# Optimization experiments

Measured on AMD Instinct MI355X. Metric: run time of the kernel, lower is better.

## Reference

```python
import jax, jax.numpy as jnp
import numpy as np

B, P, D = 16, 512, 1024   # batch, num wordpieces, bert_dim (roberta-large)
W, T, E = 400, 32, 64     # num words, num triggers (spans), num entities (spans)
H = 600                   # hidden_num of role_idn_ffn


def _make_idxs(rng, b, m, n, max_len):
    # [start, end) intervals with 0 <= start < end <= n, sorted starts per row
    starts = np.sort(rng.integers(0, n - 1, size=(b, m)), axis=1)
    ends = np.minimum(starts + rng.integers(1, max_len + 1, size=(b, m)), n)
    ends = np.maximum(ends, starts + 1)
    return np.stack([starts, ends], axis=-1).astype(np.int32)


def setup_inputs() -> dict:
    key = jax.random.key(0)
    k1, k2, k3 = jax.random.split(key, 3)
    rng = np.random.default_rng(0)
    return {
        "piece_reprs": jax.random.normal(k1, (B, P, D), dtype=jnp.float32),
        "word_idxs": jnp.asarray(_make_idxs(rng, B, W, P, 4)),
        "trigger_idxs": jnp.asarray(_make_idxs(rng, B, T, W, 8)),
        "entity_idxs": jnp.asarray(_make_idxs(rng, B, E, W, 12)),
        "W0": jax.random.normal(k2, (4 * D, H), dtype=jnp.float32) * 0.02,
        "b0": jnp.zeros((H,), dtype=jnp.float32),
        "W1": jax.random.normal(k3, (H, 2), dtype=jnp.float32) * 0.02,
        "b1": jnp.zeros((2,), dtype=jnp.float32),
    }


def _segment_mean(x, idxs):
    """Mean of x[b, start:end] per interval. x: [B,N,Dm], idxs: [B,M,2] -> [B,M,Dm].
    Vectorized replacement of the nested-loop slice+mean via inclusive prefix sums."""
    cs = jnp.concatenate([jnp.zeros_like(x[:, :1]), jnp.cumsum(x, axis=1)], axis=1)  # [B,N+1,Dm]
    s = jnp.take_along_axis(cs, idxs[:, :, 0:1], axis=1)  # [B,M,Dm]
    e = jnp.take_along_axis(cs, idxs[:, :, 1:2], axis=1)  # [B,M,Dm]
    lens = (idxs[:, :, 1] - idxs[:, :, 0]).astype(x.dtype)[:, :, None]
    return (e - s) / lens


def reference(piece_reprs, word_idxs, trigger_idxs, entity_idxs, W0, b0, W1, b1):
    # encode(): wordpiece -> word averaging (compute_word_reps_avg)
    word_reprs = _segment_mean(piece_reprs, word_idxs)          # [B, W, D]
    # scores(): span mean pooling (compute_span_reprs)
    trig = _segment_mean(word_reprs, trigger_idxs)              # [B, T, D]
    ent = _segment_mean(word_reprs, entity_idxs)                # [B, E, D]
    b, t, d = trig.shape
    e = ent.shape[1]
    # compute_binary_reprs: all (trigger, entity) pairs, trigger index varies slowly
    t_rep = jnp.broadcast_to(trig[:, :, None, :], (b, t, e, d)).reshape(b, t * e, d)
    e_rep = jnp.broadcast_to(ent[:, None, :, :], (b, t, e, d)).reshape(b, t * e, d)
    role = jnp.concatenate([t_rep, e_rep, t_rep * e_rep, jnp.abs(t_rep - e_rep)], axis=-1)  # [B,T*E,4D]
    # role_idn_ffn: Linears([4D, H, 2]) with relu between layers (dropout=0 at eval)
    h = jax.nn.relu(role @ W0 + b0)
    return h @ W1 + b1                                          # [B, T*E, 2]
```

## Files before the change

### kernel.cpp

```cpp
#include <hip/hip_runtime.h>
#include <cstddef>
#include <cstdint>

typedef float f32x4 __attribute__((ext_vector_type(4)));
typedef __bf16 bf16x8 __attribute__((ext_vector_type(8)));

constexpr int NB = 16;
constexpr int NP = 512;
constexpr int ND = 1024;
constexpr int NW = 400;
constexpr int NT = 32;
constexpr int NE = 64;
constexpr int NH = 600;
constexpr int IMGP = 128 * 64;
constexpr int IMGQ = 320 * 32;
constexpr int PREZ_N = NB * NT * NH + NB * NE * NH;

__device__ inline bf16x8 pack8(float a0, float a1, float a2, float a3,
                               float a4, float a5, float a6, float a7) {
    bf16x8 v;
    v[0] = (__bf16)a0; v[1] = (__bf16)a1; v[2] = (__bf16)a2; v[3] = (__bf16)a3;
    v[4] = (__bf16)a4; v[5] = (__bf16)a5; v[6] = (__bf16)a6; v[7] = (__bf16)a7;
    return v;
}

__device__ inline void dma16(const void* g, void* l) {
    __builtin_amdgcn_global_load_lds(
        (const __attribute__((address_space(1))) uint32_t*)g,
        (__attribute__((address_space(3))) uint32_t*)l, 16, 0, 0);
}

#define LGKM_BARRIER() \
    asm volatile("s_waitcnt lgkmcnt(0)\n\ts_barrier" ::: "memory")

template <int MAXW>
__device__ inline float4 span_mean_cols(const float* __restrict__ pbase,
                                        const int* __restrict__ wrow,
                                        int s, int e) {
    int nw = e - s;
    int ps[MAXW], pe[MAXW];
#pragma unroll
    for (int w = 0; w < MAXW; ++w) {
        bool act = w < nw;
        int ww = s + w;
        ps[w] = act ? wrow[2 * ww] : 0;
        pe[w] = act ? wrow[2 * ww + 1] : 0;
    }
    float4 acc = make_float4(0.f, 0.f, 0.f, 0.f);
#pragma unroll
    for (int w = 0; w < MAXW; ++w) {
        float4 wa = make_float4(0.f, 0.f, 0.f, 0.f);
#pragma unroll
        for (int p = 0; p < 4; ++p) {
            if (ps[w] + p < pe[w]) {
                float4 v = *(const float4*)(pbase + (size_t)(ps[w] + p) * ND);
                wa.x += v.x; wa.y += v.y; wa.z += v.z; wa.w += v.w;
            }
        }
        if (pe[w] > ps[w]) {
            float wi = 1.0f / (float)(pe[w] - ps[w]);
            acc.x += wa.x * wi; acc.y += wa.y * wi;
            acc.z += wa.z * wi; acc.w += wa.w * wi;
        }
    }
    return acc;
}

__global__ __launch_bounds__(256) void prep_kernel(
    const float* __restrict__ piece, const int* __restrict__ widx,
    const int* __restrict__ tidx, const int* __restrict__ eidx,
    const float* __restrict__ W0, __bf16* __restrict__ W0pre,
    __bf16* __restrict__ W0pair, float* __restrict__ trig,
    float* __restrict__ ent, float* __restrict__ prez,
    float* __restrict__ out, int out_size) {
    __shared__ float T[64][132];
    int id = blockIdx.x;
    int t = threadIdx.x;
    if (id < NB * (NT + NE)) {
        const int* idx;
        float* outp;
        int b;
        bool is_trig = id < NB * NT;
        if (is_trig) {
            b = id / NT; idx = tidx + id * 2; outp = trig + (size_t)id * ND;
        } else {
            int id2 = id - NB * NT;
            b = id2 / NE; idx = eidx + id2 * 2; outp = ent + (size_t)id2 * ND;
        }
        int s = idx[0], e = idx[1];
        int col = t * 4;
        const int* wrow = widx + b * NW * 2;
        const float* pbase = piece + (size_t)b * NP * ND + col;
        float4 acc = is_trig ? span_mean_cols<8>(pbase, wrow, s, e)
                             : span_mean_cols<12>(pbase, wrow, s, e);
        float inv = 1.0f / (float)(e - s);
        acc.x *= inv; acc.y *= inv; acc.z *= inv; acc.w *= inv;
        *(float4*)(outp + col) = acc;
    } else if (id < NB * (NT + NE) + 704) {
        int bid = id - NB * (NT + NE);
        if (bid < 160) {
            int kb = bid & 31, nc = bid >> 5;
            {
                int kl = t >> 2;
                int n0 = (t & 3) * 32;
                int kg = kb * 64 + kl;
                const float* src = W0 + (size_t)kg * NH + nc * 128 + n0;
#pragma unroll
                for (int g = 0; g < 8; ++g) {
                    int n = nc * 128 + n0 + g * 4;
                    float4 v = (n < NH) ? *(const float4*)(src + g * 4)
                                        : make_float4(0.f, 0.f, 0.f, 0.f);
                    *(float4*)&T[kl][n0 + g * 4] = v;
                }
            }
            __syncthreads();
#pragma unroll
            for (int s = 0; s < 4; ++s) {
                int idx = t * 4 + s;
                int row = idx >> 3, c = idx & 7;
                bf16x8 v = pack8(T[c * 8 + 0][row], T[c * 8 + 1][row],
                                 T[c * 8 + 2][row], T[c * 8 + 3][row],
                                 T[c * 8 + 4][row], T[c * 8 + 5][row],
                                 T[c * 8 + 6][row], T[c * 8 + 7][row]);
                __bf16* img = W0pre + ((size_t)nc * 32 + kb) * IMGP;
                *(bf16x8*)&img[row * 64 + ((c ^ (row & 7)) << 3)] = v;
            }
        } else if (bid < 672) {
            int e = bid - 160;
            int it = e & 63, nc = (e >> 6) & 1, zz = e >> 7;
            float (*Tp)[84] = reinterpret_cast<float(*)[84]>(&T[0][0]);
            {
                int kidx = t >> 3, part = t & 7;
                int korig = (kidx < 16) ? (2048 + it * 16 + kidx)
                                        : (3072 + it * 16 + (kidx - 16));
                const float* src = W0 + (size_t)korig * NH;
#pragma unroll
                for (int g = 0; g < 10; ++g) {
                    int n = nc * 320 + zz * 80 + part * 10 + g;
                    Tp[kidx][part * 10 + g] = (n < NH) ? src[n] : 0.0f;
                }
            }
            __syncthreads();
            __bf16* img = W0pair + ((size_t)nc * 64 + it) * IMGQ;
#pragma unroll
            for (int s = 0; s < 2; ++s) {
                int idx = s * 256 + t;
                if (idx < 320) {
                    int rloc = idx >> 2, c = idx & 3;
                    bf16x8 v = pack8(Tp[c * 8 + 0][rloc], Tp[c * 8 + 1][rloc],
                                     Tp[c * 8 + 2][rloc], Tp[c * 8 + 3][rloc],
                                     Tp[c * 8 + 4][rloc], Tp[c * 8 + 5][rloc],
                                     Tp[c * 8 + 6][rloc], Tp[c * 8 + 7][rloc]);
                    int rg = zz * 80 + rloc;
                    int slot = ((rg >> 1) + c) & 3;
                    *(bf16x8*)&img[rg * 32 + slot * 8] = v;
                }
            }
        } else {
            int j = ((bid - 672) * 256 + t) * 8;
            float4 z = make_float4(0.f, 0.f, 0.f, 0.f);
            if (j + 8 <= out_size) {
                *(float4*)(out + j) = z;
                *(float4*)(out + j + 4) = z;
            }
        }
    } else {
        int id2 = id - (NB * (NT + NE) + 704);
        int j = (id2 * 256 + t) * 8;
        float4 z = make_float4(0.f, 0.f, 0.f, 0.f);
        if (j + 8 <= PREZ_N) {
            *(float4*)(prez + j) = z;
            *(float4*)(prez + j + 4) = z;
        }
    }
}

__global__ __launch_bounds__(256) void pre_mfma_kernel(
    const float* __restrict__ trig, const float* __restrict__ ent,
    const __bf16* __restrict__ W0pre, float* __restrict__ pre_t,
    float* __restrict__ pre_e) {
    __shared__ __bf16 As[2][64 * 64];
    __shared__ __bf16 Bs[3][64 * 64];
    int mt8 = blockIdx.x, ntile = blockIdx.y, kz = blockIdx.z;
    const float* A;
    float* C;
    int kbofs, mbase;
    if (mt8 < 8) { A = trig; C = pre_t; kbofs = 0;  mbase = mt8 * 64; }
    else         { A = ent;  C = pre_e; kbofs = 16; mbase = (mt8 - 8) * 64; }
    int tid = threadIdx.x;
    int lane = tid & 63, w = tid >> 6, rw = w & 1, cw = w >> 1;
    int q = lane >> 4, l15 = lane & 15, sa = l15 & 7;
    int nc = ntile >> 1, half = ntile & 1;
    const __bf16* imgbase =
        W0pre + ((size_t)nc * 32 + kbofs) * IMGP + half * 4096;
    int ar = tid >> 2, seg = tid & 3;
    f32x4 acc[2][2] = {};
    float4 av[4];

    auto dma_bb = [&](int it, int buf) {
        const __bf16* img = imgbase + (size_t)(kz * 8 + it) * IMGP;
#pragma unroll
        for (int i = 0; i < 2; ++i) {
            int idx = i * 4 + w;
            dma16(img + idx * 512 + lane * 8, (__bf16*)Bs[buf] + idx * 512);
        }
    };
    auto load_a = [&](int it) {
        const float* src = A + (size_t)(mbase + ar) * ND + (kz * 8 + it) * 64;
#pragma unroll
        for (int i = 0; i < 2; ++i) {
            int c = seg * 2 + i;
            av[i * 2]     = *(const float4*)(src + c * 8);
            av[i * 2 + 1] = *(const float4*)(src + c * 8 + 4);
        }
    };
    auto write_a = [&](int buf) {
#pragma unroll
        for (int i = 0; i < 2; ++i) {
            int c = seg * 2 + i;
            float4 a0 = av[i * 2], a1 = av[i * 2 + 1];
            *(bf16x8*)&As[buf][ar * 64 + ((c ^ (ar & 7)) << 3)] =
                pack8(a0.x, a0.y, a0.z, a0.w, a1.x, a1.y, a1.z, a1.w);
        }
    };
    auto mfma_t = [&](int abuf, int bbuf) {
#pragma unroll
        for (int ks = 0; ks < 2; ++ks) {
            int coff = ((q ^ sa) ^ (ks << 2)) << 3;
            bf16x8 af[2];
#pragma unroll
            for (int mt = 0; mt < 2; ++mt)
                af[mt] = *(const bf16x8*)&As[abuf][(32 * rw + 16 * mt + l15) * 64 + coff];
#pragma unroll
            for (int nt = 0; nt < 2; ++nt) {
                bf16x8 bf = *(const bf16x8*)&Bs[bbuf][(32 * cw + 16 * nt + l15) * 64 + coff];
#pragma unroll
                for (int mt = 0; mt < 2; ++mt)
                    acc[mt][nt] = __builtin_amdgcn_mfma_f32_16x16x32_bf16(
                        af[mt], bf, acc[mt][nt], 0, 0, 0);
            }
        }
    };

    load_a(0);
    dma_bb(0, 0);
    dma_bb(1, 1);
    write_a(0);
    __syncthreads();

    int bc = 0, bp = 2;
    for (int it = 0; it < 8; ++it) {
        int acur = it & 1, anxt = acur ^ 1;
        if (it < 7) load_a(it + 1);
        if (it < 6) dma_bb(it + 2, bp);
        __builtin_amdgcn_s_setprio(1);
        mfma_t(acur, bc);
        __builtin_amdgcn_s_setprio(0);
        if (it < 7) write_a(anxt);
        LGKM_BARRIER();
        bc = (bc == 2) ? 0 : bc + 1;
        bp = (bp == 2) ? 0 : bp + 1;
    }

#pragma unroll
    for (int mt = 0; mt < 2; ++mt)
#pragma unroll
        for (int r = 0; r < 4; ++r) {
            float* crow =
                C + (size_t)(mbase + 32 * rw + 16 * mt + 4 * q + r) * NH;
#pragma unroll
            for (int nt = 0; nt < 2; ++nt) {
                int n = ntile * 64 + 32 * cw + 16 * nt + l15;
                if (n < NH) atomicAdd(&crow[n], acc[mt][nt][r]);
            }
        }
}

__global__ __launch_bounds__(256, 2) void pair_mfma_kernel(
    const float* __restrict__ trig, const float* __restrict__ ent,
    const __bf16* __restrict__ W0pair, const float* __restrict__ b0,
    const float* __restrict__ pre_t, const float* __restrict__ pre_e,
    const float* __restrict__ W1, const float* __restrict__ b1,
    float* __restrict__ out) {
    __shared__ __bf16 Xs[2][128 * 32];
    __shared__ __bf16 Bs[3][320 * 32];
    __shared__ __bf16 Ts[2048];
    int b = blockIdx.x, tp = blockIdx.y, nc = blockIdx.z;
    int tid = threadIdx.x;
    int lane = tid & 63, w = tid >> 6, rw = w & 1, cw = w >> 1;
    int q = lane >> 4, l15 = lane & 15;
    int xr = tid >> 1, xh = tid & 1;
    const float* t0row = trig + (size_t)(b * NT + tp * 2) * ND;
    const float* erow = ent + (size_t)(b * NE + (xr & 63)) * ND;
    const __bf16* imgbase = W0pair + (size_t)nc * 64 * IMGQ;
    f32x4 acc[4][10] = {};
    float4 ef4[2];

    auto dma_b = [&](int it, int buf) {
        const __bf16* img = imgbase + (size_t)it * IMGQ + w * 2560;
        __bf16* lds = &Bs[buf][w * 2560];
#pragma unroll
        for (int i = 0; i < 5; ++i)
            dma16(img + i * 512 + lane * 8, lds + i * 512);
    };
    auto load_e = [&](int it) {
        const float* er = erow + it * 16 + xh * 8;
        ef4[0] = *(const float4*)er;
        ef4[1] = *(const float4*)(er + 4);
    };
    auto write_x = [&](int it, int buf) {
        bf16x8 tv = *(const bf16x8*)&Ts[(xr >> 6) * 1024 + it * 16 + xh * 8];
        float tf[8], ef[8];
#pragma unroll
        for (int j = 0; j < 8; ++j) tf[j] = (float)tv[j];
        ef[0] = ef4[0].x; ef[1] = ef4[0].y; ef[2] = ef4[0].z; ef[3] = ef4[0].w;
        ef[4] = ef4[1].x; ef[5] = ef4[1].y; ef[6] = ef4[1].z; ef[7] = ef4[1].w;
        int sp = (((xr >> 1) + xh) & 3) * 8;
        int sd = (((xr >> 1) + 2 + xh) & 3) * 8;
        __bf16* xb = &Xs[buf][xr * 32];
        *(bf16x8*)(xb + sp) = pack8(
            tf[0] * ef[0], tf[1] * ef[1], tf[2] * ef[2], tf[3] * ef[3],
            tf[4] * ef[4], tf[5] * ef[5], tf[6] * ef[6], tf[7] * ef[7]);
        *(bf16x8*)(xb + sd) = pack8(
            fabsf(tf[0] - ef[0]), fabsf(tf[1] - ef[1]),
            fabsf(tf[2] - ef[2]), fabsf(tf[3] - ef[3]),
            fabsf(tf[4] - ef[4]), fabsf(tf[5] - ef[5]),
            fabsf(tf[6] - ef[6]), fabsf(tf[7] - ef[7]));
    };
    auto mfma_tile = [&](int xbuf, int bbuf) {
        const __bf16* X = Xs[xbuf];
        const __bf16* Bb = Bs[bbuf];
        bf16x8 af[4];
#pragma unroll
        for (int mt = 0; mt < 4; ++mt) {
            int r = 64 * rw + 16 * mt + l15;
            af[mt] = *(const bf16x8*)&X[r * 32 + (((r >> 1) + q) & 3) * 8];
        }
#pragma unroll
        for (int nt = 0; nt < 10; ++nt) {
            int r = 160 * cw + 16 * nt + l15;
            bf16x8 bv = *(const bf16x8*)&Bb[r * 32 + (((r >> 1) + q) & 3) * 8];
#pragma unroll
            for (int mt = 0; mt < 4; ++mt)
                acc[mt][nt] = __builtin_amdgcn_mfma_f32_16x16x32_bf16(
                    af[mt], bv, acc[mt][nt], 0, 0, 0);
        }
    };

    {
        int k0 = (tid & 127) * 8;
        const float* src = t0row + (tid >> 7) * ND + k0;
        float4 va = *(const float4*)src;
        float4 vb = *(const float4*)(src + 4);
        *(bf16x8*)&Ts[tid * 8] =
            pack8(va.x, va.y, va.z, va.w, vb.x, vb.y, vb.z, vb.w);
    }
    dma_b(0, 0);
    load_e(0);
    dma_b(1, 1);
    __syncthreads();
    write_x(0, 0);
    __syncthreads();

    int bc = 0, bp = 2;
    for (int it = 0; it < 64; ++it) {
        int xcur = it & 1, xnxt = xcur ^ 1;
        if (it < 63) load_e(it + 1);
        if (it < 62) dma_b(it + 2, bp);
        __builtin_amdgcn_s_setprio(1);
        mfma_tile(xcur, bc);
        __builtin_amdgcn_s_setprio(0);
        if (it < 63) write_x(it + 1, xnxt);
        LGKM_BARRIER();
        bc = (bc == 2) ? 0 : bc + 1;
        bp = (bp == 2) ? 0 : bp + 1;
    }

    int tglob = b * NT + tp * 2 + rw;
    const float* preT = pre_t + (size_t)tglob * NH;
    float w10[10], w11[10], b0v[10], ptv[10];
    int nbase = nc * 320 + 160 * cw + l15;
#pragma unroll
    for (int nt = 0; nt < 10; ++nt) {
        int n = nbase + 16 * nt;
        bool v = n < NH;
        w10[nt] = v ? W1[2 * n] : 0.f;
        w11[nt] = v ? W1[2 * n + 1] : 0.f;
        b0v[nt] = v ? b0[n] : 0.f;
        ptv[nt] = v ? preT[n] : 0.f;
    }
    float b10 = b1[0], b11 = b1[1];
    bool lead = (l15 == 0);
    bool addb = (nc == 0) && (cw == 0);
#pragma unroll
    for (int mt = 0; mt < 4; ++mt) {
#pragma unroll
        for (int r = 0; r < 4; ++r) {
            int e = 16 * mt + 4 * q + r;
            const float* preE = pre_e + (size_t)(b * NE + e) * NH;
            float s0 = 0.f, s1 = 0.f;
#pragma unroll
            for (int nt = 0; nt < 10; ++nt) {
                int n = nbase + 16 * nt;
                float pe = (n < NH) ? preE[n] : 0.f;
                float h = acc[mt][nt][r] + ptv[nt] + pe + b0v[nt];
                h = fmaxf(h, 0.f);
                s0 += h * w10[nt];
                s1 += h * w11[nt];
            }
#pragma unroll
            for (int m = 8; m >= 1; m >>= 1) {
                s0 += __shfl_xor(s0, m);
                s1 += __shfl_xor(s1, m);
            }
            if (lead) {
                if (addb) { s0 += b10; s1 += b11; }
                float* o = out + ((size_t)(tglob * NE + e)) * 2;
                atomicAdd(o, s0);
                atomicAdd(o + 1, s1);
            }
        }
    }
}

extern "C" void kernel_launch(void* const* d_in, const int* in_sizes, int n_in,
                              void* d_out, int out_size, void* d_ws,
                              size_t ws_size, hipStream_t stream) {
    const float* piece = (const float*)d_in[0];
    const int* widx = (const int*)d_in[1];
    const int* tidx = (const int*)d_in[2];
    const int* eidx = (const int*)d_in[3];
    const float* W0 = (const float*)d_in[4];
    const float* b0 = (const float*)d_in[5];
    const float* W1 = (const float*)d_in[6];
    const float* b1 = (const float*)d_in[7];
    float* out = (float*)d_out;

    float* ws = (float*)d_ws;
    float* trig = ws;
    float* ent = trig + (size_t)NB * NT * ND;
    float* pre_t = ent + (size_t)NB * NE * ND;
    float* pre_e = pre_t + (size_t)NB * NT * NH;
    __bf16* W0pre = (__bf16*)(pre_e + (size_t)NB * NE * NH);
    __bf16* W0pair = W0pre + (size_t)5 * 32 * IMGP;

    int nprep = NB * (NT + NE) + 704 + (PREZ_N / 2048);
    prep_kernel<<<nprep, 256, 0, stream>>>(piece, widx, tidx, eidx, W0, W0pre,
                                           W0pair, trig, ent, pre_t, out,
                                           out_size);
    pre_mfma_kernel<<<dim3(24, 10, 2), 256, 0, stream>>>(trig, ent, W0pre,
                                                         pre_t, pre_e);
    pair_mfma_kernel<<<dim3(16, 16, 2), 256, 0, stream>>>(
        trig, ent, W0pair, b0, pre_t, pre_e, W1, b1, out);
}
```

Measured before the change: 220.3 us.

## Double pair kernel block to 512 threads, halving per-wave N tile

The pair MFMA kernel now runs 512 threads (8 waves) per block instead of 256. Each wave covers 80 instead of 160 output columns, which halves the accumulator registers per wave. X-tile construction is split so each thread writes either the product or the abs-difference half, and only the first four waves issue B-tile DMAs. The goal is more waves in flight to hide latency, at the cost of more LDS A-fragment reads per MFMA and a lopsided DMA load across waves.

```diff
diff --git a/kernel.cpp b/kernel.cpp
--- a/kernel.cpp
+++ b/kernel.cpp
@@ -276,7 +276,7 @@
         }
 }
 
-__global__ __launch_bounds__(256, 2) void pair_mfma_kernel(
+__global__ __launch_bounds__(512, 4) void pair_mfma_kernel(
     const float* __restrict__ trig, const float* __restrict__ ent,
     const __bf16* __restrict__ W0pair, const float* __restrict__ b0,
     const float* __restrict__ pre_t, const float* __restrict__ pre_e,
@@ -287,45 +287,48 @@
     __shared__ __bf16 Ts[2048];
     int b = blockIdx.x, tp = blockIdx.y, nc = blockIdx.z;
     int tid = threadIdx.x;
-    int lane = tid & 63, w = tid >> 6, rw = w & 1, cw = w >> 1;
+    int lane = tid & 63, w = tid >> 6;
+    int rw = w & 1, cw = w >> 1;
     int q = lane >> 4, l15 = lane & 15;
-    int xr = tid >> 1, xh = tid & 1;
+    int xr = tid >> 2, xq = tid & 3;
     const float* t0row = trig + (size_t)(b * NT + tp * 2) * ND;
     const float* erow = ent + (size_t)(b * NE + (xr & 63)) * ND;
     const __bf16* imgbase = W0pair + (size_t)nc * 64 * IMGQ;
-    f32x4 acc[4][10] = {};
+    f32x4 acc[4][5] = {};
     float4 ef4[2];
 
     auto dma_b = [&](int it, int buf) {
-        const __bf16* img = imgbase + (size_t)it * IMGQ + w * 2560;
-        __bf16* lds = &Bs[buf][w * 2560];
-#pragma unroll
-        for (int i = 0; i < 5; ++i)
-            dma16(img + i * 512 + lane * 8, lds + i * 512);
+        if (w < 4) {
+            const __bf16* img = imgbase + (size_t)it * IMGQ + w * 2560;
+            __bf16* lds = &Bs[buf][w * 2560];
+#pragma unroll
+            for (int i = 0; i < 5; ++i)
+                dma16(img + i * 512 + lane * 8, lds + i * 512);
+        }
     };
     auto load_e = [&](int it) {
-        const float* er = erow + it * 16 + xh * 8;
+        const float* er = erow + it * 16 + (xq & 1) * 8;
         ef4[0] = *(const float4*)er;
         ef4[1] = *(const float4*)(er + 4);
     };
     auto write_x = [&](int it, int buf) {
-        bf16x8 tv = *(const bf16x8*)&Ts[(xr >> 6) * 1024 + it * 16 + xh * 8];
-        float tf[8], ef[8];
-#pragma unroll
-        for (int j = 0; j < 8; ++j) tf[j] = (float)tv[j];
+        bf16x8 tv =
+            *(const bf16x8*)&Ts[(xr >> 6) * 1024 + it * 16 + (xq & 1) * 8];
+        float ef[8];
         ef[0] = ef4[0].x; ef[1] = ef4[0].y; ef[2] = ef4[0].z; ef[3] = ef4[0].w;
         ef[4] = ef4[1].x; ef[5] = ef4[1].y; ef[6] = ef4[1].z; ef[7] = ef4[1].w;
-        int sp = (((xr >> 1) + xh) & 3) * 8;
-        int sd = (((xr >> 1) + 2 + xh) & 3) * 8;
-        __bf16* xb = &Xs[buf][xr * 32];
-        *(bf16x8*)(xb + sp) = pack8(
-            tf[0] * ef[0], tf[1] * ef[1], tf[2] * ef[2], tf[3] * ef[3],
-            tf[4] * ef[4], tf[5] * ef[5], tf[6] * ef[6], tf[7] * ef[7]);
-        *(bf16x8*)(xb + sd) = pack8(
-            fabsf(tf[0] - ef[0]), fabsf(tf[1] - ef[1]),
-            fabsf(tf[2] - ef[2]), fabsf(tf[3] - ef[3]),
-            fabsf(tf[4] - ef[4]), fabsf(tf[5] - ef[5]),
-            fabsf(tf[6] - ef[6]), fabsf(tf[7] - ef[7]));
+        bool prod = (xq < 2);
+        float vj[8];
+#pragma unroll
+        for (int j = 0; j < 8; ++j) {
+            float tf = (float)tv[j];
+            float p = tf * ef[j];
+            float d = fabsf(tf - ef[j]);
+            vj[j] = prod ? p : d;
+        }
+        int slot = (((xr >> 1) + xq) & 3) * 8;
+        *(bf16x8*)(&Xs[buf][xr * 32] + slot) =
+            pack8(vj[0], vj[1], vj[2], vj[3], vj[4], vj[5], vj[6], vj[7]);
     };
     auto mfma_tile = [&](int xbuf, int bbuf) {
         const __bf16* X = Xs[xbuf];
@@ -337,8 +340,8 @@
             af[mt] = *(const bf16x8*)&X[r * 32 + (((r >> 1) + q) & 3) * 8];
         }
 #pragma unroll
-        for (int nt = 0; nt < 10; ++nt) {
-            int r = 160 * cw + 16 * nt + l15;
+        for (int nt = 0; nt < 5; ++nt) {
+            int r = 80 * cw + 16 * nt + l15;
             bf16x8 bv = *(const bf16x8*)&Bb[r * 32 + (((r >> 1) + q) & 3) * 8];
 #pragma unroll
             for (int mt = 0; mt < 4; ++mt)
@@ -347,7 +350,7 @@
         }
     };
 
-    {
+    if (tid < 256) {
         int k0 = (tid & 127) * 8;
         const float* src = t0row + (tid >> 7) * ND + k0;
         float4 va = *(const float4*)src;
@@ -378,10 +381,10 @@
 
     int tglob = b * NT + tp * 2 + rw;
     const float* preT = pre_t + (size_t)tglob * NH;
-    float w10[10], w11[10], b0v[10], ptv[10];
-    int nbase = nc * 320 + 160 * cw + l15;
-#pragma unroll
-    for (int nt = 0; nt < 10; ++nt) {
+    float w10[5], w11[5], b0v[5], ptv[5];
+    int nbase = nc * 320 + 80 * cw + l15;
+#pragma unroll
+    for (int nt = 0; nt < 5; ++nt) {
         int n = nbase + 16 * nt;
         bool v = n < NH;
         w10[nt] = v ? W1[2 * n] : 0.f;
@@ -400,7 +403,7 @@
             const float* preE = pre_e + (size_t)(b * NE + e) * NH;
             float s0 = 0.f, s1 = 0.f;
 #pragma unroll
-            for (int nt = 0; nt < 10; ++nt) {
+            for (int nt = 0; nt < 5; ++nt) {
                 int n = nbase + 16 * nt;
                 float pe = (n < NH) ? preE[n] : 0.f;
                 float h = acc[mt][nt][r] + ptv[nt] + pe + b0v[nt];
@@ -450,6 +453,6 @@
                                            out_size);
     pre_mfma_kernel<<<dim3(24, 10, 2), 256, 0, stream>>>(trig, ent, W0pre,
                                                          pre_t, pre_e);
-    pair_mfma_kernel<<<dim3(16, 16, 2), 256, 0, stream>>>(
+    pair_mfma_kernel<<<dim3(16, 16, 2), 512, 0, stream>>>(
         trig, ent, W0pair, b0, pre_t, pre_e, W1, b1, out);
 }
```

Result: no change. 224.6 us (+1.9%).

## Shrink LDS: double-buffer pair B tiles and halve prep transpose tile

Applied to the files above, without the earlier changes.

The pair MFMA kernel moves from a three-deep B-tile ring with prefetch distance two to a plain double buffer with prefetch distance one. It also drops the s_setprio hints and uses a full __syncthreads instead of the lgkm-only barrier. The W0 transpose in the prep kernel now runs in two 32-row halves so its shared tile is half the size, and the span-mean loop is regrouped into chunks of four words. The aim is to cut LDS use so more blocks fit per CU, at the cost of less prefetch slack, so DMA latency is more exposed.

```diff
diff --git a/kernel.cpp b/kernel.cpp
--- a/kernel.cpp
+++ b/kernel.cpp
@@ -48,19 +48,23 @@
     }
     float4 acc = make_float4(0.f, 0.f, 0.f, 0.f);
 #pragma unroll
-    for (int w = 0; w < MAXW; ++w) {
-        float4 wa = make_float4(0.f, 0.f, 0.f, 0.f);
-#pragma unroll
-        for (int p = 0; p < 4; ++p) {
-            if (ps[w] + p < pe[w]) {
-                float4 v = *(const float4*)(pbase + (size_t)(ps[w] + p) * ND);
-                wa.x += v.x; wa.y += v.y; wa.z += v.z; wa.w += v.w;
-            }
-        }
-        if (pe[w] > ps[w]) {
-            float wi = 1.0f / (float)(pe[w] - ps[w]);
-            acc.x += wa.x * wi; acc.y += wa.y * wi;
-            acc.z += wa.z * wi; acc.w += wa.w * wi;
+    for (int cb = 0; cb < MAXW; cb += 4) {
+#pragma unroll
+        for (int w = cb; w < cb + 4; ++w) {
+            float4 wa = make_float4(0.f, 0.f, 0.f, 0.f);
+#pragma unroll
+            for (int p = 0; p < 4; ++p) {
+                if (ps[w] + p < pe[w]) {
+                    float4 v =
+                        *(const float4*)(pbase + (size_t)(ps[w] + p) * ND);
+                    wa.x += v.x; wa.y += v.y; wa.z += v.z; wa.w += v.w;
+                }
+            }
+            if (pe[w] > ps[w]) {
+                float wi = 1.0f / (float)(pe[w] - ps[w]);
+                acc.x += wa.x * wi; acc.y += wa.y * wi;
+                acc.z += wa.z * wi; acc.w += wa.w * wi;
+            }
         }
     }
     return acc;
@@ -73,7 +77,7 @@
     __bf16* __restrict__ W0pair, float* __restrict__ trig,
     float* __restrict__ ent, float* __restrict__ prez,
     float* __restrict__ out, int out_size) {
-    __shared__ float T[64][132];
+    __shared__ float T[32][132];
     int id = blockIdx.x;
     int t = threadIdx.x;
     if (id < NB * (NT + NE)) {
@@ -100,30 +104,34 @@
         int bid = id - NB * (NT + NE);
         if (bid < 160) {
             int kb = bid & 31, nc = bid >> 5;
-            {
-                int kl = t >> 2;
-                int n0 = (t & 3) * 32;
-                int kg = kb * 64 + kl;
-                const float* src = W0 + (size_t)kg * NH + nc * 128 + n0;
-#pragma unroll
-                for (int g = 0; g < 8; ++g) {
-                    int n = nc * 128 + n0 + g * 4;
-                    float4 v = (n < NH) ? *(const float4*)(src + g * 4)
-                                        : make_float4(0.f, 0.f, 0.f, 0.f);
-                    *(float4*)&T[kl][n0 + g * 4] = v;
+            __bf16* img = W0pre + ((size_t)nc * 32 + kb) * IMGP;
+#pragma unroll
+            for (int h = 0; h < 2; ++h) {
+                {
+                    int kl = t >> 3;
+                    int n0 = (t & 7) * 16;
+                    int kg = kb * 64 + h * 32 + kl;
+                    const float* src = W0 + (size_t)kg * NH + nc * 128 + n0;
+#pragma unroll
+                    for (int g = 0; g < 4; ++g) {
+                        int n = nc * 128 + n0 + g * 4;
+                        float4 v = (n < NH) ? *(const float4*)(src + g * 4)
+                                            : make_float4(0.f, 0.f, 0.f, 0.f);
+                        *(float4*)&T[kl][n0 + g * 4] = v;
+                    }
                 }
-            }
-            __syncthreads();
-#pragma unroll
-            for (int s = 0; s < 4; ++s) {
-                int idx = t * 4 + s;
-                int row = idx >> 3, c = idx & 7;
-                bf16x8 v = pack8(T[c * 8 + 0][row], T[c * 8 + 1][row],
-                                 T[c * 8 + 2][row], T[c * 8 + 3][row],
-                                 T[c * 8 + 4][row], T[c * 8 + 5][row],
-                                 T[c * 8 + 6][row], T[c * 8 + 7][row]);
-                __bf16* img = W0pre + ((size_t)nc * 32 + kb) * IMGP;
-                *(bf16x8*)&img[row * 64 + ((c ^ (row & 7)) << 3)] = v;
+                __syncthreads();
+#pragma unroll
+                for (int s = 0; s < 2; ++s) {
+                    int idx = s * 256 + t;
+                    int row = idx >> 2, cl = idx & 3, c = h * 4 + cl;
+                    bf16x8 v = pack8(T[cl * 8 + 0][row], T[cl * 8 + 1][row],
+                                     T[cl * 8 + 2][row], T[cl * 8 + 3][row],
+                                     T[cl * 8 + 4][row], T[cl * 8 + 5][row],
+                                     T[cl * 8 + 6][row], T[cl * 8 + 7][row]);
+                    *(bf16x8*)&img[row * 64 + ((c ^ (row & 7)) << 3)] = v;
+                }
+                __syncthreads();
             }
         } else if (bid < 672) {
             int e = bid - 160;
@@ -283,7 +291,7 @@
     const float* __restrict__ W1, const float* __restrict__ b1,
     float* __restrict__ out) {
     __shared__ __bf16 Xs[2][128 * 32];
-    __shared__ __bf16 Bs[3][320 * 32];
+    __shared__ __bf16 Bs[2][320 * 32];
     __shared__ __bf16 Ts[2048];
     int b = blockIdx.x, tp = blockIdx.y, nc = blockIdx.z;
     int tid = threadIdx.x;
@@ -327,9 +335,9 @@
             fabsf(tf[4] - ef[4]), fabsf(tf[5] - ef[5]),
             fabsf(tf[6] - ef[6]), fabsf(tf[7] - ef[7]));
     };
-    auto mfma_tile = [&](int xbuf, int bbuf) {
-        const __bf16* X = Xs[xbuf];
-        const __bf16* Bb = Bs[bbuf];
+    auto mfma_tile = [&](int buf) {
+        const __bf16* X = Xs[buf];
+        const __bf16* Bb = Bs[buf];
         bf16x8 af[4];
 #pragma unroll
         for (int mt = 0; mt < 4; ++mt) {
@@ -357,23 +365,19 @@
     }
     dma_b(0, 0);
     load_e(0);
-    dma_b(1, 1);
     __syncthreads();
     write_x(0, 0);
     __syncthreads();
 
-    int bc = 0, bp = 2;
     for (int it = 0; it < 64; ++it) {
-        int xcur = it & 1, xnxt = xcur ^ 1;
-        if (it < 63) load_e(it + 1);
-        if (it < 62) dma_b(it + 2, bp);
-        __builtin_amdgcn_s_setprio(1);
-        mfma_tile(xcur, bc);
-        __builtin_amdgcn_s_setprio(0);
-        if (it < 63) write_x(it + 1, xnxt);
-        LGKM_BARRIER();
-        bc = (bc == 2) ? 0 : bc + 1;
-        bp = (bp == 2) ? 0 : bp + 1;
+        int cur = it & 1, nxt = cur ^ 1;
+        if (it < 63) {
+            load_e(it + 1);
+            dma_b(it + 1, nxt);
+        }
+        mfma_tile(cur);
+        if (it < 63) write_x(it + 1, nxt);
+        __syncthreads();
     }
 
     int tglob = b * NT + tp * 2 + rw;
```

After: 216.7 us. About the same (-1.6%).
